# Performance work log

Measured on AMD Instinct MI355X. Metric: run time of the kernel, lower is better.

Reference implementation:

```python
import jax, jax.numpy as jnp
import numpy as np
from jax.ops import segment_sum, segment_max

N, D, B = 1536, 32, 8            # nodes, candidate out-degree per node, sequential batch steps
OBS, HID, HEADS, C = 33, 64, 4, 8  # obs_dim, GRU hidden, attn heads, out_dim//heads
E = N * D


def setup_inputs() -> dict:
    key = jax.random.key(0)
    ks = jax.random.split(key, 16)
    g = lambda i, shape, s=0.1: jax.random.normal(ks[i], shape, jnp.float32) * s
    src = jnp.repeat(jnp.arange(N), D)                    # uniform degree -> scatter_topk = row top-k
    dst = jax.random.randint(ks[0], (E,), 0, N)
    return dict(
        H_t=jax.random.normal(ks[1], (B, N, OBS), jnp.float32),
        src=src, dst=dst, k=4,
        W_e1=g(2, (OBS, 32)), b_e1=jnp.zeros(32), W_e2=g(3, (32, 32)), b_e2=jnp.zeros(32),
        ln_g=jnp.ones(32), ln_b=jnp.zeros(32),
        W_ih=g(4, (3 * HID, 32)), W_hh=g(5, (3 * HID, HID)),
        b_ih=jnp.zeros(3 * HID), b_hh=jnp.zeros(3 * HID),
        W_s1=g(6, (2 * HID, 64)), b_s1=jnp.zeros(64), W_s2=g(7, (64, 1)), b_s2=jnp.zeros(1),
        W_gat=g(8, (HID, HEADS * C)), att_src=g(9, (HEADS, C)), att_dst=g(10, (HEADS, C)),
        b_gat=jnp.zeros(HEADS * C),
    )


def _layernorm(x, g, b, eps=1e-5):
    mu = x.mean(-1, keepdims=True)
    var = ((x - mu) ** 2).mean(-1, keepdims=True)
    return (x - mu) * jax.lax.rsqrt(var + eps) * g + b


def _forward(H_t, src, dst, k, W_e1, b_e1, W_e2, b_e2, ln_g, ln_b,
             W_ih, W_hh, b_ih, b_hh, W_s1, b_s1, W_s2, b_s2,
             W_gat, att_src, att_dst, b_gat):
    # ObsEmbedding: Linear-ReLU-Linear-ReLU-LayerNorm, applied to all (B,N) at once
    x = jax.nn.relu(H_t @ W_e1 + b_e1)
    x = jax.nn.relu(x @ W_e2 + b_e2)
    H_emb = _layernorm(x, ln_g, ln_b)              # (B,N,32)

    def step(h, e_t):
        # --- NodeMemory: shared GRUCell, h carried across batch steps ---
        gi = e_t @ W_ih.T + b_ih                   # (N,3H)
        gh = h @ W_hh.T + b_hh
        i_r, i_z, i_n = jnp.split(gi, 3, -1)
        h_r, h_z, h_n = jnp.split(gh, 3, -1)
        r = jax.nn.sigmoid(i_r + h_r)
        z = jax.nn.sigmoid(i_z + h_z)
        n = jnp.tanh(i_n + r * h_n)
        h_new = (1.0 - z) * n + z * h              # (N,HID)

        # --- EdgeScorer: sigmoid MLP score per candidate edge, keep top-k per source ---
        feat = jnp.concatenate([h_new[src], h_new[dst]], -1)        # (E,2*HID)
        score = jax.nn.sigmoid(
            (jax.nn.relu(feat @ W_s1 + b_s1) @ W_s2 + b_s2)[:, 0])  # (E,)
        s2 = score.reshape(N, D)
        top_idx = jax.lax.top_k(s2, k)[1]                           # (N,k)
        keep = (jnp.zeros((N, D), bool)
                .at[jnp.arange(N)[:, None], top_idx].set(True)).reshape(-1)  # (E,)
        w = jnp.where(keep, score, 0.0)                             # soft edge weights

        # --- GATConv (add_self_loops=False), pruned edges masked out of the softmax ---
        xh = (h_new @ W_gat).reshape(N, HEADS, C)
        a_s = (xh * att_src).sum(-1)               # (N,HEADS)
        a_d = (xh * att_dst).sum(-1)
        logit = jax.nn.leaky_relu(a_s[src] + a_d[dst], 0.2)         # (E,HEADS)
        logit = jnp.where(keep[:, None], logit, -1e30)
        m = segment_max(logit, dst, num_segments=N)                 # softmax grouped by target
        ex = jnp.where(keep[:, None], jnp.exp(logit - m[dst]), 0.0)
        ssum = segment_sum(ex, dst, num_segments=N)
        alpha = ex / jnp.clip(ssum[dst], 1e-16)                     # (E,HEADS)

        msg = alpha[:, :, None] * xh[src] * w[:, None, None]        # edge_weight scales messages
        out = segment_sum(msg, dst, num_segments=N).reshape(N, HEADS * C) + b_gat

        # --- densify attention: scatter-accumulate then row-normalize ---
        A = jnp.zeros((HEADS, N, N), alpha.dtype).at[:, src, dst].add(alpha.T)
        A = A / jnp.clip(A.sum(-1, keepdims=True), 1e-9)
        return h_new, (out, A)

    h0 = jnp.zeros((N, HID), H_t.dtype)
    _, (outs, attns) = jax.lax.scan(step, h0, H_emb)
    return outs, attns                              # (B,N,32), (B,HEADS,N,N)


def reference(H_t, src, dst, k, W_e1, b_e1, W_e2, b_e2, ln_g, ln_b,
              W_ih, W_hh, b_ih, b_hh, W_s1, b_s1, W_s2, b_s2,
              W_gat, att_src, att_dst, b_gat):
    return _forward(H_t, src, dst, k, W_e1, b_e1, W_e2, b_e2, ln_g, ln_b,
                    W_ih, W_hh, b_ih, b_hh, W_s1, b_s1, W_s2, b_s2,
                    W_gat, att_src, att_dst, b_gat)
```

## Files before the change

kernel.cpp:

```cpp
#include <hip/hip_runtime.h>
#include <math.h>

#define NN   1536
#define DG   32
#define BB   8
#define OBSD 33
#define HID  64
#define NHEAD 4
#define EE   (NN*DG)

__device__ __forceinline__ float sigm(float x){ return 1.0f/(1.0f+expf(-x)); }

__global__ void __launch_bounds__(256) k_embgi(
                      const float* __restrict__ Ht,
                      const float* __restrict__ We1, const float* __restrict__ be1,
                      const float* __restrict__ We2, const float* __restrict__ be2,
                      const float* __restrict__ lng, const float* __restrict__ lnb,
                      const float* __restrict__ Wih, const float* __restrict__ bih,
                      float* __restrict__ GI, int* __restrict__ cursor){
    __shared__ float lwih[192*33];
    int tid = threadIdx.x;
    if(blockIdx.x < 6) cursor[blockIdx.x*256 + tid] = 0;
    for(int i=tid;i<192*32;i+=256){ int r=i>>5, c=i&31; lwih[r*33+c]=Wih[i]; }
    __syncthreads();
    int lane = tid & 63;
    int j32 = lane & 31;
    int bn = blockIdx.x*4 + (tid>>6);
    const float* hrow = Ht + (size_t)bn*OBSD;
    float x1 = be1[j32];
    for(int o=0;o<OBSD;o++) x1 += hrow[o]*We1[o*32+j32];
    x1 = fmaxf(x1,0.f);
    float x2 = be2[j32];
    for(int i=0;i<32;i++){
        float xi = __shfl(x1, (lane & 32) | i, 64);
        x2 += xi * We2[i*32+j32];
    }
    x2 = fmaxf(x2,0.f);
    float mu = x2;
    for(int m=16;m>=1;m>>=1) mu += __shfl_xor(mu, m, 32);
    mu *= (1.0f/32.0f);
    float d = x2-mu; float var = d*d;
    for(int m=16;m>=1;m>>=1) var += __shfl_xor(var, m, 32);
    var *= (1.0f/32.0f);
    float xln = d*rsqrtf(var+1e-5f)*lng[j32]+lnb[j32];
    int j = lane;
    float gr=bih[j], gz=bih[64+j], gn=bih[128+j];
    for(int kk=0;kk<32;kk++){
        float ek = __shfl(xln, kk, 64);
        gr += ek*lwih[j*33+kk];
        gz += ek*lwih[(64+j)*33+kk];
        gn += ek*lwih[(128+j)*33+kk];
    }
    float* g = GI + (size_t)bn*192;
    g[j]=gr; g[64+j]=gz; g[128+j]=gn;
}

__global__ void k_count(const int* __restrict__ dst, int* __restrict__ cursor){
    int e = blockIdx.x*256+threadIdx.x;
    if(e<EE) atomicAdd(&cursor[dst[e]],1);
}
__global__ void k_scan(int* __restrict__ cnt, int* __restrict__ indptr){
    __shared__ int part[256];
    int t = threadIdx.x;
    int local[6]; int s=0;
    for(int i=0;i<6;i++){ local[i]=cnt[t*6+i]; s+=local[i]; }
    part[t]=s; __syncthreads();
    if(t==0){ int acc=0; for(int i=0;i<256;i++){ int v=part[i]; part[i]=acc; acc+=v; } }
    __syncthreads();
    int pre = part[t];
    for(int i=0;i<6;i++){ int idx=t*6+i; indptr[idx]=pre; cnt[idx]=pre; pre+=local[i]; }
    if(t==255) indptr[NN]=EE;
}
__global__ void k_fill(const int* __restrict__ dst, int* __restrict__ cursor, int* __restrict__ eids){
    int e = blockIdx.x*256+threadIdx.x;
    if(e<EE){ int p = atomicAdd(&cursor[dst[e]],1); eids[p]=e; }
}

__global__ void __launch_bounds__(384) k_gru_all(const float* __restrict__ GI,
                       const float* __restrict__ Whh, const float* __restrict__ bhh,
                       float* __restrict__ Hall){
    __shared__ float lw[192*65];
    int tid = threadIdx.x;
    for(int i=tid;i<192*64;i+=384){ int r=i>>6, c=i&63; lw[r*65+c]=Whh[i]; }
    __syncthreads();
    int node = blockIdx.x*6 + (tid>>6);
    int j = tid&63;
    float b_r=bhh[j], b_z=bhh[64+j], b_n=bhh[128+j];
    const float* lwr = lw + j*65;
    const float* lwz = lw + (64+j)*65;
    const float* lwn = lw + (128+j)*65;
    float hold = 0.f;
    for(int t=0;t<BB;t++){
        float hr=b_r, hz=b_z, hn=b_n;
        for(int kk=0;kk<64;kk++){
            float hk = __shfl(hold,kk);
            hr += hk*lwr[kk];
            hz += hk*lwz[kk];
            hn += hk*lwn[kk];
        }
        const float* g = GI + ((size_t)t*NN+node)*192;
        float r  = sigm(g[j]     + hr);
        float z  = sigm(g[64+j]  + hz);
        float nn_= tanhf(g[128+j] + r*hn);
        hold = (1.f-z)*nn_ + z*hold;
        Hall[((size_t)t*NN+node)*64 + j] = hold;
    }
}

__global__ void __launch_bounds__(256) k_post(const float* __restrict__ Hall,
                       const float* __restrict__ Ws1, const float* __restrict__ Wgat,
                       const float* __restrict__ atts, const float* __restrict__ attd,
                       float* __restrict__ P, float* __restrict__ Q,
                       float* __restrict__ xh, float* __restrict__ as_, float* __restrict__ ad_){
    __shared__ float ws1l[128*64];
    __shared__ float wgl[64*32];
    int tid = threadIdx.x;
    for(int i=tid;i<128*64;i+=256) ws1l[i]=Ws1[i];
    for(int i=tid;i<64*32;i+=256)  wgl[i]=Wgat[i];
    __syncthreads();
    int bn = blockIdx.x*4 + (tid>>6);
    int j = tid&63;
    float hv = Hall[(size_t)bn*64+j];
    float p=0.f,q=0.f,xv=0.f;
    for(int kk=0;kk<64;kk++){
        float hk=__shfl(hv,kk);
        p += hk*ws1l[kk*64+j];
        q += hk*ws1l[(64+kk)*64+j];
        if(j<32) xv += hk*wgl[kk*32+j];
    }
    P[(size_t)bn*64+j]=p; Q[(size_t)bn*64+j]=q;
    if(j<32){
        xh[(size_t)bn*32+j]=xv;
        float asv = xv*atts[j];
        float adv = xv*attd[j];
        for(int m=1;m<8;m<<=1){ asv += __shfl_xor(asv,m); adv += __shfl_xor(adv,m); }
        if((j&7)==0){ as_[(size_t)bn*4+(j>>3)]=asv; ad_[(size_t)bn*4+(j>>3)]=adv; }
    }
}

__global__ void __launch_bounds__(256) k_edge(const float* __restrict__ P, const float* __restrict__ Q,
                       const float* __restrict__ bs1, const float* __restrict__ Ws2,
                       const float* __restrict__ bs2, const int* __restrict__ dst,
                       const int* __restrict__ kptr, float* __restrict__ wbuf){
    int tid = threadIdx.x;
    int t = blockIdx.y;
    int row = blockIdx.x*8 + (tid>>5);
    int d = tid & 31;
    int e = row*DG + d;
    int de = dst[e];
    const float4* Pr = (const float4*)(P + ((size_t)t*NN+row)*64);
    const float4* Qr = (const float4*)(Q + ((size_t)t*NN+de)*64);
    const float4* B1 = (const float4*)bs1;
    const float4* W2 = (const float4*)Ws2;
    float acc = 0.f;
    #pragma unroll
    for(int jj=0;jj<16;jj++){
        float4 pv=Pr[jj], qv=Qr[jj], bv=B1[jj], wv=W2[jj];
        acc += fmaxf(pv.x+qv.x+bv.x,0.f)*wv.x;
        acc += fmaxf(pv.y+qv.y+bv.y,0.f)*wv.y;
        acc += fmaxf(pv.z+qv.z+bv.z,0.f)*wv.z;
        acc += fmaxf(pv.w+qv.w+bv.w,0.f)*wv.w;
    }
    float score = sigm(acc + bs2[0]);
    int kk = kptr[0]; if(kk>32) kk=32; if(kk<0) kk=0;
    bool sel=false;
    for(int it=0; it<kk; it++){
        float v = sel ? -INFINITY : score;
        int idx = d;
        for(int m=16;m>=1;m>>=1){
            float ov = __shfl_xor(v,m,32);
            int   oi = __shfl_xor(idx,m,32);
            if(ov>v || (ov==v && oi<idx)){ v=ov; idx=oi; }
        }
        if(idx==d) sel=true;
    }
    wbuf[(size_t)t*EE + e] = sel ? score : 0.f;
}

__global__ void __launch_bounds__(256) k_soft(const int* __restrict__ indptr, const int* __restrict__ eids,
                       const float* __restrict__ as_, const float* __restrict__ ad_,
                       const float* __restrict__ wbuf, const float* __restrict__ xhb,
                       const float* __restrict__ bgat,
                       float* __restrict__ alphab, float* __restrict__ outp){
    int n = blockIdx.x;
    int t = blockIdx.y;
    int h = threadIdx.x>>6;
    int lane = threadIdx.x&63;
    const float* w     = wbuf  + (size_t)t*EE;
    const float* asb   = as_   + (size_t)t*NN*4;
    const float* xhbt  = xhb   + (size_t)t*NN*32;
    float*       alpha = alphab+ (size_t)t*EE*4;
    int beg = indptr[n], end = indptr[n+1];
    int deg = end-beg;
    float adv = ad_[((size_t)t*NN+n)*4+h];
    float acc[8];
    #pragma unroll
    for(int c=0;c<8;c++) acc[c]=0.f;
    if(deg<=64){
        bool valid = lane<deg;
        int e = valid ? eids[beg+lane] : 0;
        float we = valid ? w[e] : 0.f;
        bool kept = we>0.f;
        int s = e>>5;
        float lg = -INFINITY, ex = 0.f;
        if(kept){
            lg = asb[s*4+h]+adv;
            lg = lg>0.f ? lg : 0.2f*lg;
        }
        float m = lg;
        for(int mm=32;mm>=1;mm>>=1) m = fmaxf(m,__shfl_xor(m,mm));
        if(kept) ex = expf(lg-m);
        float ssum = ex;
        for(int mm=32;mm>=1;mm>>=1) ssum += __shfl_xor(ssum,mm);
        float inv = 1.0f/fmaxf(ssum,1e-16f);
        if(kept){
            float a = ex*inv;
            alpha[e*4+h] = a;
            float aw = a*we;
            const float4* xr = (const float4*)(xhbt + s*32 + h*8);
            float4 x0 = xr[0], x1 = xr[1];
            acc[0]+=aw*x0.x; acc[1]+=aw*x0.y; acc[2]+=aw*x0.z; acc[3]+=aw*x0.w;
            acc[4]+=aw*x1.x; acc[5]+=aw*x1.y; acc[6]+=aw*x1.z; acc[7]+=aw*x1.w;
        }
    } else {
        float m = -INFINITY;
        for(int i=beg+lane;i<end;i+=64){
            int e = eids[i];
            if(w[e]>0.f){
                float lg = asb[(e>>5)*4+h]+adv;
                lg = lg>0.f ? lg : 0.2f*lg;
                m = fmaxf(m,lg);
            }
        }
        for(int mm=32;mm>=1;mm>>=1) m = fmaxf(m,__shfl_xor(m,mm));
        float ssum=0.f;
        for(int i=beg+lane;i<end;i+=64){
            int e = eids[i];
            float ex = 0.f;
            if(w[e]>0.f){
                float lg = asb[(e>>5)*4+h]+adv;
                lg = lg>0.f ? lg : 0.2f*lg;
                ex = expf(lg-m);
            }
            alpha[e*4+h]=ex;
            ssum += ex;
        }
        for(int mm=32;mm>=1;mm>>=1) ssum += __shfl_xor(ssum,mm);
        float inv = 1.0f/fmaxf(ssum,1e-16f);
        for(int i=beg+lane;i<end;i+=64){
            int e = eids[i];
            if(w[e]>0.f){
                float a = alpha[e*4+h]*inv;
                alpha[e*4+h]=a;
                float aw = a*w[e];
                const float* xr = xhbt + (e>>5)*32 + h*8;
                #pragma unroll
                for(int c=0;c<8;c++) acc[c] += aw*xr[c];
            }
        }
    }
    for(int mm=32;mm>=1;mm>>=1){
        #pragma unroll
        for(int c=0;c<8;c++) acc[c] += __shfl_xor(acc[c],mm);
    }
    if(lane==0){
        float* o = outp + ((size_t)t*NN+n)*32 + h*8;
        float4 o0 = { acc[0]+bgat[h*8+0], acc[1]+bgat[h*8+1], acc[2]+bgat[h*8+2], acc[3]+bgat[h*8+3] };
        float4 o1 = { acc[4]+bgat[h*8+4], acc[5]+bgat[h*8+5], acc[6]+bgat[h*8+6], acc[7]+bgat[h*8+7] };
        ((float4*)o)[0]=o0; ((float4*)o)[1]=o1;
    }
}

__global__ void __launch_bounds__(256) k_scatter(const float* __restrict__ alphab,
                       const float* __restrict__ wbuf,
                       const int* __restrict__ dst, float* __restrict__ attn){
    __shared__ int   kde[DG];
    __shared__ float kan[DG][NHEAD];
    __shared__ int   scnt;
    int n = blockIdx.x;
    int t = blockIdx.y;
    int tid = threadIdx.x;
    const float* alpha = alphab + (size_t)t*EE*4;
    const float* w     = wbuf   + (size_t)t*EE;
    if(tid<64){
        int d = tid;
        int e = n*DG + d;
        bool kept = false;
        if(d<DG) kept = (w[e] > 0.f);
        unsigned long long mask = __ballot(kept);
        float4 av = {0.f,0.f,0.f,0.f};
        int de = 0;
        if(kept){ de = dst[e]; av = *(const float4*)(alpha + (size_t)e*4); }
        float s0=av.x, s1=av.y, s2=av.z, s3=av.w;
        for(int m=32;m>=1;m>>=1){
            s0 += __shfl_xor(s0,m); s1 += __shfl_xor(s1,m);
            s2 += __shfl_xor(s2,m); s3 += __shfl_xor(s3,m);
        }
        if(kept){
            int pos = __popcll(mask & ((1ull<<d)-1ull));
            kde[pos] = de;
            kan[pos][0] = av.x / fmaxf(s0,1e-9f);
            kan[pos][1] = av.y / fmaxf(s1,1e-9f);
            kan[pos][2] = av.z / fmaxf(s2,1e-9f);
            kan[pos][3] = av.w / fmaxf(s3,1e-9f);
        }
        if(tid==0) scnt = __popcll(mask);
    }
    __syncthreads();
    int cnt = scnt;
    size_t base = (size_t)t*NHEAD*NN*NN + (size_t)n*NN;
    #pragma unroll
    for(int it=0; it<6; it++){
        int c = it*256 + tid;
        int h = c/(NN/4), c4 = c%(NN/4);
        float4 f4 = {0.f,0.f,0.f,0.f};
        for(int p=0;p<cnt;p++){
            int de = kde[p];
            if((de>>2)==c4) ((float*)&f4)[de&3] += kan[p][h];
        }
        ((float4*)(attn + base + (size_t)h*NN*NN))[c4] = f4;
    }
}

extern "C" void kernel_launch(void* const* d_in, const int* in_sizes, int n_in,
                              void* d_out, int out_size, void* d_ws, size_t ws_size,
                              hipStream_t stream) {
    const float* Ht   = (const float*)d_in[0];
    const int*   dst  = (const int*)  d_in[2];
    const int*   kptr = (const int*)  d_in[3];
    const float* We1  = (const float*)d_in[4];
    const float* be1  = (const float*)d_in[5];
    const float* We2  = (const float*)d_in[6];
    const float* be2  = (const float*)d_in[7];
    const float* lng  = (const float*)d_in[8];
    const float* lnb  = (const float*)d_in[9];
    const float* Wih  = (const float*)d_in[10];
    const float* Whh  = (const float*)d_in[11];
    const float* bih  = (const float*)d_in[12];
    const float* bhh  = (const float*)d_in[13];
    const float* Ws1  = (const float*)d_in[14];
    const float* bs1  = (const float*)d_in[15];
    const float* Ws2  = (const float*)d_in[16];
    const float* bs2  = (const float*)d_in[17];
    const float* Wgat = (const float*)d_in[18];
    const float* atts = (const float*)d_in[19];
    const float* attd = (const float*)d_in[20];
    const float* bgat = (const float*)d_in[21];

    float* outp = (float*)d_out;
    float* attn = outp + (size_t)BB*NN*32;

    float* ws    = (float*)d_ws;
    float* GI    = ws;
    float* Hall  = ws + 2359296;
    float* P     = ws + 3145728;
    float* Q     = ws + 3932160;
    float* xh    = ws + 4718592;
    float* as_   = ws + 5111808;
    float* ad_   = ws + 5160960;
    float* wbuf  = ws + 5210112;
    float* alpha = ws + 5603328;
    int*   ibase = (int*)(ws + 7176192);
    int*   cursor= ibase;
    int*   indptr= ibase + 2048;
    int*   eids  = ibase + 4096;

    k_embgi<<<BB*NN/4, 256, 0, stream>>>(Ht, We1, be1, We2, be2, lng, lnb, Wih, bih, GI, cursor);
    k_count<<<EE/256, 256, 0, stream>>>(dst, cursor);
    k_scan<<<1, 256, 0, stream>>>(cursor, indptr);
    k_fill<<<EE/256, 256, 0, stream>>>(dst, cursor, eids);
    k_gru_all<<<NN/6, 384, 0, stream>>>(GI, Whh, bhh, Hall);
    k_post<<<BB*NN/4, 256, 0, stream>>>(Hall, Ws1, Wgat, atts, attd, P, Q, xh, as_, ad_);
    {
        dim3 ge(NN/8, BB);
        k_edge<<<ge, 256, 0, stream>>>(P, Q, bs1, Ws2, bs2, dst, kptr, wbuf);
        dim3 g(NN, BB);
        k_soft<<<g, 256, 0, stream>>>(indptr, eids, as_, ad_, wbuf, xh, bgat, alpha, outp);
        k_scatter<<<g, 256, 0, stream>>>(alpha, wbuf, dst, attn);
    }
}
```

Before: 536.4 us.

## Split GRU hidden matvec across two waves per node and broadcast via LDS

The GRU kernel now assigns two wavefronts to each node, each computing half of the 64-long recurrent dot product. Partial sums and the hidden state are exchanged through shared memory with block barriers, which doubles the grid and halves the serial chain per step. The post kernel also replaces cross-lane shuffles with LDS broadcast reads of the hidden vector. In exchange there are three block-wide syncs per time step and an extra Whh load per block. The post kernel has no barrier between writing hb and reading it, which is only safe because each node's row lives within a single wave.

Result: no change. 537.9 us (+0.3%).

```diff
diff --git a/kernel.cpp b/kernel.cpp
--- a/kernel.cpp
+++ b/kernel.cpp
@@ -76,34 +76,52 @@
     if(e<EE){ int p = atomicAdd(&cursor[dst[e]],1); eids[p]=e; }
 }
 
-__global__ void __launch_bounds__(384) k_gru_all(const float* __restrict__ GI,
+__global__ void __launch_bounds__(384) k_gru2(const float* __restrict__ GI,
                        const float* __restrict__ Whh, const float* __restrict__ bhh,
                        float* __restrict__ Hall){
     __shared__ float lw[192*65];
+    __shared__ float hb[3][64];
+    __shared__ float part[3][2][192];
     int tid = threadIdx.x;
     for(int i=tid;i<192*64;i+=384){ int r=i>>6, c=i&63; lw[r*65+c]=Whh[i]; }
+    int wv = tid>>6;
+    int nl = wv>>1;
+    int half = wv&1;
+    int j = tid&63;
+    int node = blockIdx.x*3 + nl;
+    if(half==0) hb[nl][j] = 0.f;
     __syncthreads();
-    int node = blockIdx.x*6 + (tid>>6);
-    int j = tid&63;
     float b_r=bhh[j], b_z=bhh[64+j], b_n=bhh[128+j];
     const float* lwr = lw + j*65;
     const float* lwz = lw + (64+j)*65;
     const float* lwn = lw + (128+j)*65;
-    float hold = 0.f;
+    int kb = half*32;
     for(int t=0;t<BB;t++){
-        float hr=b_r, hz=b_z, hn=b_n;
-        for(int kk=0;kk<64;kk++){
-            float hk = __shfl(hold,kk);
+        float hr=0.f, hz=0.f, hn=0.f;
+        for(int kk=kb;kk<kb+32;kk++){
+            float hk = hb[nl][kk];
             hr += hk*lwr[kk];
             hz += hk*lwz[kk];
             hn += hk*lwn[kk];
         }
+        part[nl][half][j]     = hr;
+        part[nl][half][64+j]  = hz;
+        part[nl][half][128+j] = hn;
+        __syncthreads();
+        float hrT = part[nl][0][j]     + part[nl][1][j]     + b_r;
+        float hzT = part[nl][0][64+j]  + part[nl][1][64+j]  + b_z;
+        float hnT = part[nl][0][128+j] + part[nl][1][128+j] + b_n;
         const float* g = GI + ((size_t)t*NN+node)*192;
-        float r  = sigm(g[j]     + hr);
-        float z  = sigm(g[64+j]  + hz);
-        float nn_= tanhf(g[128+j] + r*hn);
-        hold = (1.f-z)*nn_ + z*hold;
-        Hall[((size_t)t*NN+node)*64 + j] = hold;
+        float r  = sigm(g[j]     + hrT);
+        float z  = sigm(g[64+j]  + hzT);
+        float nn_= tanhf(g[128+j] + r*hnT);
+        float hnew = (1.f-z)*nn_ + z*hb[nl][j];
+        __syncthreads();
+        if(half==0){
+            hb[nl][j] = hnew;
+            Hall[((size_t)t*NN+node)*64 + j] = hnew;
+        }
+        __syncthreads();
     }
 }
 
@@ -114,16 +132,18 @@
                        float* __restrict__ xh, float* __restrict__ as_, float* __restrict__ ad_){
     __shared__ float ws1l[128*64];
     __shared__ float wgl[64*32];
+    __shared__ float hb[4][64];
     int tid = threadIdx.x;
     for(int i=tid;i<128*64;i+=256) ws1l[i]=Ws1[i];
     for(int i=tid;i<64*32;i+=256)  wgl[i]=Wgat[i];
     __syncthreads();
-    int bn = blockIdx.x*4 + (tid>>6);
+    int nl = tid>>6;
+    int bn = blockIdx.x*4 + nl;
     int j = tid&63;
-    float hv = Hall[(size_t)bn*64+j];
+    hb[nl][j] = Hall[(size_t)bn*64+j];
     float p=0.f,q=0.f,xv=0.f;
     for(int kk=0;kk<64;kk++){
-        float hk=__shfl(hv,kk);
+        float hk = hb[nl][kk];
         p += hk*ws1l[kk*64+j];
         q += hk*ws1l[(64+kk)*64+j];
         if(j<32) xv += hk*wgl[kk*32+j];
@@ -369,7 +389,7 @@
     k_count<<<EE/256, 256, 0, stream>>>(dst, cursor);
     k_scan<<<1, 256, 0, stream>>>(cursor, indptr);
     k_fill<<<EE/256, 256, 0, stream>>>(dst, cursor, eids);
-    k_gru_all<<<NN/6, 384, 0, stream>>>(GI, Whh, bhh, Hall);
+    k_gru2<<<NN/3, 384, 0, stream>>>(GI, Whh, bhh, Hall);
     k_post<<<BB*NN/4, 256, 0, stream>>>(Hall, Ws1, Wgat, atts, attd, P, Q, xh, as_, ad_);
     {
         dim3 ge(NN/8, BB);
```
